# Optimization experiments

Measured on AMD Instinct MI355X. Metric: run time of the kernel, lower is better.

## Reference

```python
import jax, jax.numpy as jnp
import numpy as np

TAU = 1.0
M_OUT = 32  # max_out_node_size
NEG = -1e30


def setup_inputs() -> dict:
    key = jax.random.key(0)
    B, H, U, maxN = 64, 512, 512, 512
    M = M_OUT
    in_size = H + M - 1
    lengths_np = np.where(np.arange(B) % 2 == 0, 256, 512).astype(np.int32)
    total = int(lengths_np.sum())  # 24576
    ks = jax.random.split(key, 14)
    h = jax.random.normal(ks[0], (total, H), jnp.float32)
    hg = jax.random.normal(ks[1], (B, H), jnp.float32)
    u = jax.random.uniform(ks[2], (M, B, maxN), jnp.float32, 1e-20, 1.0)
    gumbel = -jnp.log(-jnp.log(u))
    s = lambda k, shp, fan: jax.random.normal(k, shp, jnp.float32) * (fan ** -0.5)
    return {
        'h': h, 'hg': hg,
        'lengths': jnp.asarray(lengths_np),
        'gumbel': gumbel,
        'W1': s(ks[3], (U, H), H),
        'W2': s(ks[4], (U, H), H),
        'wc': s(ks[5], (U, 1), 1),
        'v': s(ks[6], (1, U), U),
        'w_ih': s(ks[7], (3 * H, in_size), in_size),
        'w_hh': s(ks[8], (3 * H, H), H),
        'b_ih': s(ks[9], (3 * H,), in_size),
        'b_hh': s(ks[10], (3 * H,), in_size),
        'Wf': s(ks[11], (M - 1, H), H),
        'bf': s(ks[12], (M - 1,), H),
    }


def _gru_cell(x, hprev, w_ih, w_hh, b_ih, b_hh):
    H = hprev.shape[-1]
    gi = x @ w_ih.T + b_ih
    gh = hprev @ w_hh.T + b_hh
    r = jax.nn.sigmoid(gi[:, :H] + gh[:, :H])
    z = jax.nn.sigmoid(gi[:, H:2 * H] + gh[:, H:2 * H])
    n = jnp.tanh(gi[:, 2 * H:] + r * gh[:, 2 * H:])
    return (1.0 - z) * n + z * hprev


def reference(h, hg, lengths, gumbel, W1, W2, wc, v, w_ih, w_hh, b_ih, b_hh, Wf, bf):
    B = lengths.shape[0]
    M, _, maxN = gumbel.shape
    H = hg.shape[1]
    total = h.shape[0]
    # pad_sequence: ragged h -> [B, maxN, H], zero-padded
    offsets = jnp.concatenate([jnp.zeros((1,), lengths.dtype), jnp.cumsum(lengths)[:-1]])
    pos = jnp.arange(maxN)
    mask = pos[None, :] < lengths[:, None]                      # [B, maxN]
    idx = jnp.clip(offsets[:, None] + pos[None, :], 0, total - 1)
    enc = h[idx] * mask[..., None].astype(h.dtype)              # [B, maxN, H]
    enc_proj = jnp.einsum('bnh,uh->bnu', enc, W1)               # W1(encoder_out), hoisted
    wc_vec = wc[:, 0]
    v_vec = v[0]
    theta_pos = jnp.arange(M - 1)

    def step(carry, xs):
        dec_in, hid, cov, closs = carry
        g, i = xs
        hid = _gru_cell(dec_in, hid, w_ih, w_hh, b_ih, b_hh)
        uj = jnp.tanh(enc_proj + (hid @ W2.T)[:, None, :] + cov[:, :, None] * wc_vec)
        scores = jnp.einsum('bnu,u->bn', uj, v_vec)
        att = jax.nn.softmax(jnp.where(mask, scores, NEG), axis=-1)  # [B, maxN]
        closs = closs + jnp.minimum(att, cov).sum()
        cov = cov + att
        # gumbel-softmax (hard, straight-through) over nodes
        y = jax.nn.softmax((jnp.log(att + 1e-12) + g) / TAU, axis=1)
        y_hard = jax.nn.one_hot(jnp.argmax(y, axis=1), maxN, dtype=y.dtype)
        att_hard = y_hard + y - jax.lax.stop_gradient(y)
        chosen = jnp.einsum('bnh,bn->bh', enc, att_hard)
        theta = jax.nn.sigmoid(hid @ Wf.T + bf) * (theta_pos < i).astype(hid.dtype)
        dec_in = jnp.concatenate([chosen, theta], axis=1)
        return (dec_in, hid, cov, closs), (att_hard, theta)

    dec_in0 = jnp.zeros((B, H + M - 1), h.dtype)
    cov0 = jnp.zeros((B, maxN), h.dtype)
    carry0 = (dec_in0, hg, cov0, jnp.asarray(0.0, h.dtype))
    (_, _, _, closs), (ptrs, thetas) = jax.lax.scan(step, carry0, (gumbel, jnp.arange(M)))
    pointer = jnp.transpose(ptrs, (1, 2, 0))   # [B, maxN, M]
    adj = jnp.transpose(thetas, (1, 2, 0))     # [B, M-1, M]
    return pointer, closs / B, enc, adj
```

## Files before the change

kernel.cpp:

```cpp
#include <hip/hip_runtime.h>
#include <math.h>

#define B 64
#define H 512
#define MAXN 512
#define U 512
#define MM 32
#define IN_SZ 543
#define DEC_STRIDE 544

#define PTR_OFF 0
#define PTR_SZ (B*MAXN*MM)
#define CLOSS_OFF (PTR_OFF + PTR_SZ)
#define ENC_OFF (CLOSS_OFF + 1)
#define ENC_SZ (B*MAXN*H)
#define ADJ_OFF (ENC_OFF + ENC_SZ)

#define EP_OFF 0
#define EP_SZ (B*MAXN*U)
#define GP_OFF (EP_OFF + EP_SZ)
#define GP_SZ (4*3*B*H)
#define HID0_OFF (GP_OFF + GP_SZ)
#define HID1_OFF (HID0_OFF + B*H)
#define W2H_OFF  (HID1_OFF + B*H)
#define COV_OFF  (W2H_OFF + B*H)
#define SC_OFF   (COV_OFF + B*MAXN)
#define DEC_OFF  (SC_OFF + B*MAXN)
#define CL_OFF   (DEC_OFF + B*DEC_STRIDE)
#define OFFS_OFF (CL_OFF + 64)
#define W1H_OFF  (OFFS_OFF + 64)
#define W1L_OFF  (W1H_OFF + 131072)

typedef short bf16x8 __attribute__((ext_vector_type(8)));
typedef float f32x4  __attribute__((ext_vector_type(4)));

__device__ __forceinline__ float tanh_fast(float x){
    float e = __builtin_amdgcn_exp2f(x * 2.885390081777927f);
    return 1.0f - 2.0f * __builtin_amdgcn_rcpf(e + 1.0f);
}

__device__ __forceinline__ unsigned short f2bf(float x){
    unsigned int u = __float_as_uint(x);
    u = (u + 0x7fffu + ((u >> 16) & 1u)) >> 16;
    return (unsigned short)u;
}

__global__ void k_init(float* __restrict__ ws, float* __restrict__ out,
                       const float* __restrict__ hg, const int* __restrict__ lengths,
                       const float* __restrict__ W1){
    int gid = blockIdx.x*256 + threadIdx.x;
    int nth = gridDim.x*256;
    float* ptr = out + PTR_OFF;
    for (int i=gid;i<PTR_SZ;i+=nth) ptr[i]=0.f;
    float* dec = ws + DEC_OFF;
    for (int i=gid;i<B*DEC_STRIDE;i+=nth) dec[i]=0.f;
    float* cov = ws + COV_OFF;
    float* hid0 = ws + HID0_OFF;
    for (int i=gid;i<B*H;i+=nth){ cov[i]=0.f; hid0[i]=hg[i]; }
    unsigned short* w1h = (unsigned short*)(ws + W1H_OFF);
    unsigned short* w1l = (unsigned short*)(ws + W1L_OFF);
    for (int i=gid;i<512*512;i+=nth){
        float x = W1[i];
        unsigned short hb = f2bf(x);
        float hf = __uint_as_float(((unsigned int)hb)<<16);
        w1h[i] = hb;
        w1l[i] = f2bf(x - hf);
    }
    if (gid<64) (ws+CL_OFF)[gid]=0.f;
    if (gid==0){
        int* offs=(int*)(ws+OFFS_OFF); int acc=0;
        for(int b=0;b<B;b++){ offs[b]=acc; acc+=lengths[b]; }
    }
}

__global__ __launch_bounds__(256) void k_gather(const float* __restrict__ h,
        const int* __restrict__ lengths, const float* __restrict__ offs_f,
        float* __restrict__ enc){
    const int* offs = (const int*)offs_f;
    int t = threadIdx.x;
    int row = blockIdx.x*2 + (t>>7);
    int c = (t&127)*4;
    int b = row >> 9, n = row & 511;
    int len = lengths[b];
    float4 v = make_float4(0.f,0.f,0.f,0.f);
    if (n < len){
        const float* p = h + (size_t)(offs[b]+n)*H + c;
        v = *(const float4*)p;
    }
    float* q = enc + (size_t)row*H + c;
    q[0]=v.x; q[1]=v.y; q[2]=v.z; q[3]=v.w;
}

__global__ __launch_bounds__(256) void k_gemm_mfma(const float* __restrict__ enc,
        const unsigned short* __restrict__ w1h, const unsigned short* __restrict__ w1l,
        float* __restrict__ ep){
    __shared__ unsigned short sAH[128][40];
    __shared__ unsigned short sAL[128][40];
    __shared__ unsigned short sBH[128][40];
    __shared__ unsigned short sBL[128][40];
    int tid = threadIdx.x;
    int bm = blockIdx.x >> 2, bn = blockIdx.x & 3;
    int r0 = bm*128, u0 = bn*128;
    int wid = tid>>6, lane = tid&63;
    int wr = wid>>1, wc = wid&1;
    int lr = lane&15, lk = (lane>>4)*8;
    f32x4 acc[4][4];
#pragma unroll
    for (int i=0;i<4;i++)
#pragma unroll
        for (int j=0;j<4;j++) acc[i][j] = (f32x4){0.f,0.f,0.f,0.f};
    int rowA = tid>>2, seg = tid&3;
    for (int k0=0;k0<512;k0+=32){
#pragma unroll
        for (int half=0; half<2; ++half){
            int row = rowA + half*64;
            const float* asrc = &enc[(size_t)(r0+row)*512 + k0 + seg*8];
            bf16x8 vh, vl;
#pragma unroll
            for (int j=0;j<8;j++){
                float x = asrc[j];
                unsigned short hb = f2bf(x);
                float hf = __uint_as_float(((unsigned int)hb)<<16);
                vh[j] = (short)hb;
                vl[j] = (short)f2bf(x - hf);
            }
            *(bf16x8*)&sAH[row][seg*8] = vh;
            *(bf16x8*)&sAL[row][seg*8] = vl;
            size_t bidx = (size_t)(u0+row)*512 + k0 + seg*8;
            *(bf16x8*)&sBH[row][seg*8] = *(const bf16x8*)&w1h[bidx];
            *(bf16x8*)&sBL[row][seg*8] = *(const bf16x8*)&w1l[bidx];
        }
        __syncthreads();
        bf16x8 aH[4], aL[4], bH[4], bL[4];
#pragma unroll
        for (int f=0; f<4; f++){
            aH[f] = *(const bf16x8*)&sAH[wr*64+f*16+lr][lk];
            aL[f] = *(const bf16x8*)&sAL[wr*64+f*16+lr][lk];
            bH[f] = *(const bf16x8*)&sBH[wc*64+f*16+lr][lk];
            bL[f] = *(const bf16x8*)&sBL[wc*64+f*16+lr][lk];
        }
#pragma unroll
        for (int mf=0;mf<4;mf++){
#pragma unroll
            for (int nf=0;nf<4;nf++){
                acc[mf][nf] = __builtin_amdgcn_mfma_f32_16x16x32_bf16(aH[mf], bH[nf], acc[mf][nf], 0,0,0);
                acc[mf][nf] = __builtin_amdgcn_mfma_f32_16x16x32_bf16(aH[mf], bL[nf], acc[mf][nf], 0,0,0);
                acc[mf][nf] = __builtin_amdgcn_mfma_f32_16x16x32_bf16(aL[mf], bH[nf], acc[mf][nf], 0,0,0);
            }
        }
        __syncthreads();
    }
#pragma unroll
    for (int mf=0;mf<4;mf++){
#pragma unroll
        for (int nf=0;nf<4;nf++){
#pragma unroll
            for (int r=0;r<4;r++){
                int row = r0 + wr*64 + mf*16 + (lane>>4)*4 + r;
                int col = u0 + wc*64 + nf*16 + lr;
                ep[(size_t)row*512 + col] = acc[mf][nf][r];
            }
        }
    }
}

__global__ __launch_bounds__(256) void k_gruP(const float* __restrict__ dec_in,
        const float* __restrict__ hid_in,
        const float* __restrict__ w_ih, const float* __restrict__ w_hh,
        float* __restrict__ gp){
    __shared__ float As[64][36];
    __shared__ float Ws[12][36];
    int tid=threadIdx.x, b=tid&63, q=tid>>6;
    int s = blockIdx.x >> 7;
    int h0 = (int)(blockIdx.x & 127) * 4;
    const float* xs; int xstride, kbeg, kend; const float* W; int wstride;
    if (s==0){ xs=dec_in; xstride=DEC_STRIDE; kbeg=0;   kend=288;   W=w_ih; wstride=IN_SZ; }
    else if(s==1){ xs=dec_in; xstride=DEC_STRIDE; kbeg=288; kend=IN_SZ; W=w_ih; wstride=IN_SZ; }
    else if(s==2){ xs=hid_in; xstride=512; kbeg=0;   kend=256; W=w_hh; wstride=512; }
    else         { xs=hid_in; xstride=512; kbeg=256; kend=512; W=w_hh; wstride=512; }
    float a0=0.f,a1=0.f,a2=0.f;
    for (int k0=kbeg; k0<kend; k0+=32){
        for (int it=0;it<2;it++){
            int idx=tid+it*256; int row=idx>>3, c=idx&7; int k=k0+c*4;
            float4 v=make_float4(0.f,0.f,0.f,0.f);
            const float* p=&xs[row*xstride+k];
            if (k+3 < kend) v=*(const float4*)p;
            else { if(k<kend)v.x=p[0]; if(k+1<kend)v.y=p[1]; if(k+2<kend)v.z=p[2]; }
            *(float4*)&As[row][c*4]=v;
        }
        if (tid<96){
            int rr=tid>>3, c=tid&7; int g=rr>>2, qq=rr&3;
            int j=g*512 + h0+qq; int k=k0+c*4;
            float4 v=make_float4(0.f,0.f,0.f,0.f);
            const float* p=&W[(size_t)j*wstride+k];
            if (wstride==512){
                v=*(const float4*)p;
            } else {
                if(k<kend)v.x=p[0]; if(k+1<kend)v.y=p[1];
                if(k+2<kend)v.z=p[2]; if(k+3<kend)v.w=p[3];
            }
            *(float4*)&Ws[rr][c*4]=v;
        }
        __syncthreads();
#pragma unroll
        for (int kk=0;kk<32;kk+=4){
            float4 a=*(const float4*)&As[b][kk];
            float4 w0=*(const float4*)&Ws[q][kk];
            float4 w1=*(const float4*)&Ws[4+q][kk];
            float4 w2=*(const float4*)&Ws[8+q][kk];
            a0 += a.x*w0.x + a.y*w0.y + a.z*w0.z + a.w*w0.w;
            a1 += a.x*w1.x + a.y*w1.y + a.z*w1.z + a.w*w1.w;
            a2 += a.x*w2.x + a.y*w2.y + a.z*w2.z + a.w*w2.w;
        }
        __syncthreads();
    }
    int h = h0 + q;
    gp[((s*3+0)*64+b)*512 + h] = a0;
    gp[((s*3+1)*64+b)*512 + h] = a1;
    gp[((s*3+2)*64+b)*512 + h] = a2;
}

__global__ __launch_bounds__(512) void k_mid(const float* __restrict__ gp,
        const float* __restrict__ hid_in, float* __restrict__ hid_out,
        const float* __restrict__ b_ih, const float* __restrict__ b_hh,
        const float* __restrict__ W2, const float* __restrict__ Wf,
        const float* __restrict__ bf,
        float* __restrict__ w2h, float* __restrict__ dec_in,
        float* __restrict__ adj, int step){
    __shared__ float sH[512];
    int b = blockIdx.x >> 2, uc = blockIdx.x & 3;
    int tid = threadIdx.x;
    {
        int h = tid;
        float gI0 = gp[((0*3+0)*64+b)*512+h] + gp[((1*3+0)*64+b)*512+h];
        float gI1 = gp[((0*3+1)*64+b)*512+h] + gp[((1*3+1)*64+b)*512+h];
        float gI2 = gp[((0*3+2)*64+b)*512+h] + gp[((1*3+2)*64+b)*512+h];
        float gH0 = gp[((2*3+0)*64+b)*512+h] + gp[((3*3+0)*64+b)*512+h];
        float gH1 = gp[((2*3+1)*64+b)*512+h] + gp[((3*3+1)*64+b)*512+h];
        float gH2 = gp[((2*3+2)*64+b)*512+h] + gp[((3*3+2)*64+b)*512+h];
        float gi0=gI0+b_ih[h],     gh0=gH0+b_hh[h];
        float gi1=gI1+b_ih[512+h], gh1=gH1+b_hh[512+h];
        float gi2=gI2+b_ih[1024+h],gh2=gH2+b_hh[1024+h];
        float r=1.f/(1.f+expf(-(gi0+gh0)));
        float z=1.f/(1.f+expf(-(gi1+gh1)));
        float nn=tanhf(gi2 + r*gh2);
        float hv=(1.f-z)*nn + z*hid_in[b*512+h];
        sH[h]=hv;
        if (uc==0) hid_out[b*512+h]=hv;
    }
    __syncthreads();
    int wv=tid>>6, lane=tid&63;
    for (int ul=wv; ul<128; ul+=8){
        int u = uc*128 + ul;
        const float* wr = &W2[(size_t)u*512];
        float acc=0.f;
#pragma unroll
        for (int t=0;t<8;t++){ int k=t*64+lane; acc += wr[k]*sH[k]; }
#pragma unroll
        for (int m=1;m<64;m<<=1) acc += __shfl_xor(acc, m, 64);
        if (lane==0) w2h[b*512+u]=acc;
    }
    if (uc==0){
        for (int ul=wv; ul<31; ul+=8){
            const float* wr = &Wf[(size_t)ul*512];
            float acc=0.f;
#pragma unroll
            for (int t=0;t<8;t++){ int k=t*64+lane; acc += wr[k]*sH[k]; }
#pragma unroll
            for (int m=1;m<64;m<<=1) acc += __shfl_xor(acc, m, 64);
            if (lane==0){
                float th = 1.f/(1.f+expf(-(acc + bf[ul])));
                th = (ul < step) ? th : 0.f;
                dec_in[b*DEC_STRIDE + 512 + ul] = th;
                adj[b*992 + ul*32 + step] = th;
            }
        }
    }
}

__global__ __launch_bounds__(256) void k_scores(const float* __restrict__ ep,
        const float* __restrict__ w2h, const float* __restrict__ cov,
        const float* __restrict__ wc, const float* __restrict__ v,
        const int* __restrict__ lengths, float* __restrict__ sc){
    __shared__ float sW[512], sV[512], sC[512];
    int b = blockIdx.x >> 4, nc = blockIdx.x & 15;
    int len = lengths[b];
    if (nc*32 >= len) return;
    int tid=threadIdx.x;
    for (int idx=tid; idx<384; idx+=256){
        int which = idx>>7, c = (idx&127)*4;
        float4 val;
        if (which==0) val=*(const float4*)&w2h[b*512+c];
        else if (which==1) val=*(const float4*)&v[c];
        else val=*(const float4*)&wc[c];
        float* dst = (which==0)?sW:((which==1)?sV:sC);
        *(float4*)&dst[c]=val;
    }
    __syncthreads();
    int wv=tid>>6, lane=tid&63;
    float4 vv0=*(const float4*)&sV[lane*8], vv1=*(const float4*)&sV[lane*8+4];
    float4 cc0=*(const float4*)&sC[lane*8], cc1=*(const float4*)&sC[lane*8+4];
    float4 ww0=*(const float4*)&sW[lane*8], ww1=*(const float4*)&sW[lane*8+4];
#pragma unroll
    for (int r=0;r<8;r++){
        int n = nc*32 + wv*8 + r;
        float cb = cov[b*512+n];
        const float4* rr = (const float4*)&ep[((size_t)b*512+n)*512 + lane*8];
        float4 e0=rr[0], e1=rr[1];
        float acc;
        acc  = tanh_fast(e0.x + ww0.x + cb*cc0.x)*vv0.x;
        acc += tanh_fast(e0.y + ww0.y + cb*cc0.y)*vv0.y;
        acc += tanh_fast(e0.z + ww0.z + cb*cc0.z)*vv0.z;
        acc += tanh_fast(e0.w + ww0.w + cb*cc0.w)*vv0.w;
        acc += tanh_fast(e1.x + ww1.x + cb*cc1.x)*vv1.x;
        acc += tanh_fast(e1.y + ww1.y + cb*cc1.y)*vv1.y;
        acc += tanh_fast(e1.z + ww1.z + cb*cc1.z)*vv1.z;
        acc += tanh_fast(e1.w + ww1.w + cb*cc1.w)*vv1.w;
#pragma unroll
        for (int m=1;m<64;m<<=1) acc += __shfl_xor(acc, m, 64);
        if (lane==0) sc[b*512+n]=acc;
    }
}

__global__ __launch_bounds__(512) void k_soft(const float* __restrict__ sc,
        const float* __restrict__ gum, const int* __restrict__ lengths,
        const float* __restrict__ enc, float* __restrict__ cov,
        float* __restrict__ dec_in, float* __restrict__ closs_b,
        float* __restrict__ pointer, int step){
    __shared__ float red[512];
    __shared__ int  redi[512];
    int b=blockIdx.x, n=threadIdx.x;
    int len=lengths[b];
    float e = (n<len)? expf(sc[b*512+n]) : 0.f;
    red[n]=e; __syncthreads();
    for(int o=256;o>=1;o>>=1){ if(n<o) red[n]+=red[n+o]; __syncthreads(); }
    float Z=red[0]; __syncthreads();
    float att=e/Z;
    float c=cov[b*512+n];
    red[n]=fminf(att,c); __syncthreads();
    for(int o=256;o>=1;o>>=1){ if(n<o) red[n]+=red[n+o]; __syncthreads(); }
    if(n==0) closs_b[b]+=red[0];
    __syncthreads();
    cov[b*512+n]=c+att;
    float lg=logf(att+1e-12f)+gum[((size_t)step*64+b)*512+n];
    red[n]=lg; redi[n]=n; __syncthreads();
    for(int o=256;o>=1;o>>=1){
        if(n<o && red[n+o]>red[n]){ red[n]=red[n+o]; redi[n]=redi[n+o]; }
        __syncthreads();
    }
    int ns=redi[0];
    if(n==0) pointer[b*16384 + ns*32 + step]=1.f;
    dec_in[b*DEC_STRIDE+n]=enc[((size_t)b*512+ns)*512+n];
}

__global__ void k_final(const float* __restrict__ closs_b, float* __restrict__ out){
    if (threadIdx.x==0 && blockIdx.x==0){
        float s=0.f;
        for(int b=0;b<B;b++) s+=closs_b[b];
        out[CLOSS_OFF]=s/64.f;
    }
}

extern "C" void kernel_launch(void* const* d_in, const int* in_sizes, int n_in,
                              void* d_out, int out_size, void* d_ws, size_t ws_size,
                              hipStream_t stream){
    const float* h      = (const float*)d_in[0];
    const float* hg     = (const float*)d_in[1];
    const int*   lengths= (const int*)  d_in[2];
    const float* gumbel = (const float*)d_in[3];
    const float* W1     = (const float*)d_in[4];
    const float* W2     = (const float*)d_in[5];
    const float* wc     = (const float*)d_in[6];
    const float* v      = (const float*)d_in[7];
    const float* w_ih   = (const float*)d_in[8];
    const float* w_hh   = (const float*)d_in[9];
    const float* b_ih   = (const float*)d_in[10];
    const float* b_hh   = (const float*)d_in[11];
    const float* Wf     = (const float*)d_in[12];
    const float* bf     = (const float*)d_in[13];
    float* out = (float*)d_out;
    float* ws  = (float*)d_ws;
    float* enc = out + ENC_OFF;
    float* adj = out + ADJ_OFF;
    float* pointer = out + PTR_OFF;
    float* ep   = ws + EP_OFF;
    float* gp   = ws + GP_OFF;
    float* hidA = ws + HID0_OFF;
    float* hidB = ws + HID1_OFF;
    float* w2h  = ws + W2H_OFF;
    float* cov  = ws + COV_OFF;
    float* sc   = ws + SC_OFF;
    float* dec  = ws + DEC_OFF;
    float* clb  = ws + CL_OFF;
    const unsigned short* w1h = (const unsigned short*)(ws + W1H_OFF);
    const unsigned short* w1l = (const unsigned short*)(ws + W1L_OFF);

    hipLaunchKernelGGL(k_init,     dim3(512),  dim3(256), 0, stream, ws, out, hg, lengths, W1);
    hipLaunchKernelGGL(k_gather,   dim3(16384),dim3(256), 0, stream, h, lengths, ws+OFFS_OFF, enc);
    hipLaunchKernelGGL(k_gemm_mfma,dim3(1024), dim3(256), 0, stream, enc, w1h, w1l, ep);

    for (int i=0;i<MM;i++){
        const float* hin = (i&1)? hidB : hidA;
        float*       hout= (i&1)? hidA : hidB;
        hipLaunchKernelGGL(k_gruP,   dim3(512),  dim3(256), 0, stream,
                           dec, hin, w_ih, w_hh, gp);
        hipLaunchKernelGGL(k_mid,    dim3(256),  dim3(512), 0, stream,
                           gp, hin, hout, b_ih, b_hh, W2, Wf, bf, w2h, dec, adj, i);
        hipLaunchKernelGGL(k_scores, dim3(1024), dim3(256), 0, stream,
                           ep, w2h, cov, wc, v, lengths, sc);
        hipLaunchKernelGGL(k_soft,   dim3(64),   dim3(512), 0, stream,
                           sc, gumbel, lengths, enc, cov, dec, clb, pointer, i);
    }
    hipLaunchKernelGGL(k_final, dim3(1), dim3(64), 0, stream, clb, out);
}
```

Before: 1.732 ms.

## Fuse gumbel argmax and coverage update into next step's GRU projection kernel

Moves the per-step softmax/gumbel argmax, coverage update and pointer write from a separate kernel into the following iteration's GRU input-projection kernel. Each input-side block redundantly recomputes the selected node for all batch rows and gathers the chosen encoder row and theta directly into shared memory, removing the dec_in buffer. This cuts one kernel launch per decoding step at the cost of duplicated reduction work and extra score/gumbel reads per block. The last step's selection is handled by a single trailing launch of the old kernel.

```diff
diff --git a/kernel.cpp b/kernel.cpp
--- a/kernel.cpp
+++ b/kernel.cpp
@@ -26,7 +26,8 @@
 #define COV_OFF  (W2H_OFF + B*H)
 #define SC_OFF   (COV_OFF + B*MAXN)
 #define DEC_OFF  (SC_OFF + B*MAXN)
-#define CL_OFF   (DEC_OFF + B*DEC_STRIDE)
+#define TH_OFF   (DEC_OFF + B*DEC_STRIDE)
+#define CL_OFF   (TH_OFF + B*32)
 #define OFFS_OFF (CL_OFF + 64)
 #define W1H_OFF  (OFFS_OFF + 64)
 #define W1L_OFF  (W1H_OFF + 131072)
@@ -52,8 +53,6 @@
     int nth = gridDim.x*256;
     float* ptr = out + PTR_OFF;
     for (int i=gid;i<PTR_SZ;i+=nth) ptr[i]=0.f;
-    float* dec = ws + DEC_OFF;
-    for (int i=gid;i<B*DEC_STRIDE;i+=nth) dec[i]=0.f;
     float* cov = ws + COV_OFF;
     float* hid0 = ws + HID0_OFF;
     for (int i=gid;i<B*H;i+=nth){ cov[i]=0.f; hid0[i]=hg[i]; }
@@ -164,29 +163,109 @@
     }
 }
 
-__global__ __launch_bounds__(256) void k_gruP(const float* __restrict__ dec_in,
+__global__ __launch_bounds__(256) void k_gruPS(
         const float* __restrict__ hid_in,
         const float* __restrict__ w_ih, const float* __restrict__ w_hh,
-        float* __restrict__ gp){
+        const float* __restrict__ sc, const float* __restrict__ gum,
+        const int* __restrict__ lengths, const float* __restrict__ enc,
+        const float* __restrict__ th, float* __restrict__ cov,
+        float* __restrict__ clb, float* __restrict__ pointer,
+        float* __restrict__ gp, int step){
     __shared__ float As[64][36];
     __shared__ float Ws[12][36];
+    __shared__ float red[256];
+    __shared__ int   sNs[64];
+    __shared__ float sZ[64];
     int tid=threadIdx.x, b=tid&63, q=tid>>6;
     int s = blockIdx.x >> 7;
-    int h0 = (int)(blockIdx.x & 127) * 4;
-    const float* xs; int xstride, kbeg, kend; const float* W; int wstride;
-    if (s==0){ xs=dec_in; xstride=DEC_STRIDE; kbeg=0;   kend=288;   W=w_ih; wstride=IN_SZ; }
-    else if(s==1){ xs=dec_in; xstride=DEC_STRIDE; kbeg=288; kend=IN_SZ; W=w_ih; wstride=IN_SZ; }
-    else if(s==2){ xs=hid_in; xstride=512; kbeg=0;   kend=256; W=w_hh; wstride=512; }
-    else         { xs=hid_in; xstride=512; kbeg=256; kend=512; W=w_hh; wstride=512; }
+    int hc = blockIdx.x & 127;
+    int h0 = hc * 4;
+
+    if (s < 2 && step > 0){
+        int wv = tid>>6, lane = tid&63;
+        for (int bb=wv; bb<64; bb+=4){
+            int len = lengths[bb];
+            const float* scb = &sc[bb*512];
+            const float* gb  = &gum[((size_t)(step-1)*64+bb)*512];
+            float e[8]; float zs=0.f;
+#pragma unroll
+            for (int c=0;c<8;c++){
+                int n = c*64 + lane;
+                float ev = (n<len)? expf(scb[n]) : 0.f;
+                e[c]=ev; zs += ev;
+            }
+#pragma unroll
+            for (int m=1;m<64;m<<=1) zs += __shfl_xor(zs, m, 64);
+            float best=-1e38f; int bi=0;
+#pragma unroll
+            for (int c=0;c<8;c++){
+                int n = c*64 + lane;
+                float lg = logf(e[c]/zs + 1e-12f) + gb[n];
+                if (lg > best){ best=lg; bi=n; }
+            }
+#pragma unroll
+            for (int m=1;m<64;m<<=1){
+                float ob = __shfl_xor(best, m, 64);
+                int   oi = __shfl_xor(bi, m, 64);
+                if (ob > best || (ob==best && oi<bi)){ best=ob; bi=oi; }
+            }
+            if (lane==0){ sNs[bb]=bi; sZ[bb]=zs; }
+        }
+        __syncthreads();
+        if (s==0 && hc < 64){
+            int bb = hc;
+            int len = lengths[bb];
+            float Z = sZ[bb];
+            int n0=tid, n1=tid+256;
+            float e0=(n0<len)? expf(sc[bb*512+n0]) : 0.f;
+            float e1=(n1<len)? expf(sc[bb*512+n1]) : 0.f;
+            float a0=e0/Z, a1=e1/Z;
+            float c0=cov[bb*512+n0], c1=cov[bb*512+n1];
+            red[tid]=fminf(a0,c0)+fminf(a1,c1); __syncthreads();
+            for(int o=128;o>=1;o>>=1){ if(tid<o) red[tid]+=red[tid+o]; __syncthreads(); }
+            if(tid==0){
+                clb[bb] += red[0];
+                pointer[bb*16384 + sNs[bb]*32 + (step-1)] = 1.f;
+            }
+            cov[bb*512+n0]=c0+a0;
+            cov[bb*512+n1]=c1+a1;
+            __syncthreads();
+        }
+    }
+
+    int kbeg, kend; const float* W; int wstride;
+    if (s==0){ kbeg=0;   kend=288;   W=w_ih; wstride=IN_SZ; }
+    else if(s==1){ kbeg=288; kend=IN_SZ; W=w_ih; wstride=IN_SZ; }
+    else if(s==2){ kbeg=0;   kend=256; W=w_hh; wstride=512; }
+    else         { kbeg=256; kend=512; W=w_hh; wstride=512; }
     float a0=0.f,a1=0.f,a2=0.f;
     for (int k0=kbeg; k0<kend; k0+=32){
-        for (int it=0;it<2;it++){
-            int idx=tid+it*256; int row=idx>>3, c=idx&7; int k=k0+c*4;
-            float4 v=make_float4(0.f,0.f,0.f,0.f);
-            const float* p=&xs[row*xstride+k];
-            if (k+3 < kend) v=*(const float4*)p;
-            else { if(k<kend)v.x=p[0]; if(k+1<kend)v.y=p[1]; if(k+2<kend)v.z=p[2]; }
-            *(float4*)&As[row][c*4]=v;
+        if (s < 2){
+            for (int it=0;it<2;it++){
+                int idx=tid+it*256; int row=idx>>3, c=idx&7; int k=k0+c*4;
+                float vx0=0.f, vx1=0.f, vx2=0.f, vx3=0.f;
+                if (step > 0){
+                    int nsr = sNs[row];
+                    const float* er = &enc[((size_t)(row*512 + nsr))*512];
+                    const float* tr = &th[row*32];
+#pragma unroll
+                    for (int j=0;j<4;j++){
+                        int kk = k + j;
+                        float val;
+                        if (kk < 512) val = er[kk];
+                        else if (kk < IN_SZ) val = tr[kk-512];
+                        else val = 0.f;
+                        if (j==0) vx0=val; else if(j==1) vx1=val;
+                        else if (j==2) vx2=val; else vx3=val;
+                    }
+                }
+                *(float4*)&As[row][c*4]=make_float4(vx0,vx1,vx2,vx3);
+            }
+        } else {
+            for (int it=0;it<2;it++){
+                int idx=tid+it*256; int row=idx>>3,c=idx&7; int k=k0+c*4;
+                *(float4*)&As[row][c*4] = *(const float4*)&hid_in[row*512+k];
+            }
         }
         if (tid<96){
             int rr=tid>>3, c=tid&7; int g=rr>>2, qq=rr&3;
@@ -225,7 +304,7 @@
         const float* __restrict__ b_ih, const float* __restrict__ b_hh,
         const float* __restrict__ W2, const float* __restrict__ Wf,
         const float* __restrict__ bf,
-        float* __restrict__ w2h, float* __restrict__ dec_in,
+        float* __restrict__ w2h, float* __restrict__ th,
         float* __restrict__ adj, int step){
     __shared__ float sH[512];
     int b = blockIdx.x >> 2, uc = blockIdx.x & 3;
@@ -269,10 +348,10 @@
 #pragma unroll
             for (int m=1;m<64;m<<=1) acc += __shfl_xor(acc, m, 64);
             if (lane==0){
-                float th = 1.f/(1.f+expf(-(acc + bf[ul])));
-                th = (ul < step) ? th : 0.f;
-                dec_in[b*DEC_STRIDE + 512 + ul] = th;
-                adj[b*992 + ul*32 + step] = th;
+                float thv = 1.f/(1.f+expf(-(acc + bf[ul])));
+                thv = (ul < step) ? thv : 0.f;
+                th[b*32 + ul] = thv;
+                adj[b*992 + ul*32 + step] = thv;
             }
         }
     }
@@ -391,6 +470,7 @@
     float* cov  = ws + COV_OFF;
     float* sc   = ws + SC_OFF;
     float* dec  = ws + DEC_OFF;
+    float* th   = ws + TH_OFF;
     float* clb  = ws + CL_OFF;
     const unsigned short* w1h = (const unsigned short*)(ws + W1H_OFF);
     const unsigned short* w1l = (const unsigned short*)(ws + W1L_OFF);
@@ -402,14 +482,15 @@
     for (int i=0;i<MM;i++){
         const float* hin = (i&1)? hidB : hidA;
         float*       hout= (i&1)? hidA : hidB;
-        hipLaunchKernelGGL(k_gruP,   dim3(512),  dim3(256), 0, stream,
-                           dec, hin, w_ih, w_hh, gp);
+        hipLaunchKernelGGL(k_gruPS,  dim3(512),  dim3(256), 0, stream,
+                           hin, w_ih, w_hh, sc, gumbel, lengths, enc, th,
+                           cov, clb, pointer, gp, i);
         hipLaunchKernelGGL(k_mid,    dim3(256),  dim3(512), 0, stream,
-                           gp, hin, hout, b_ih, b_hh, W2, Wf, bf, w2h, dec, adj, i);
+                           gp, hin, hout, b_ih, b_hh, W2, Wf, bf, w2h, th, adj, i);
         hipLaunchKernelGGL(k_scores, dim3(1024), dim3(256), 0, stream,
                            ep, w2h, cov, wc, v, lengths, sc);
-        hipLaunchKernelGGL(k_soft,   dim3(64),   dim3(512), 0, stream,
-                           sc, gumbel, lengths, enc, cov, dec, clb, pointer, i);
-    }
-    hipLaunchKernelGGL(k_final, dim3(1), dim3(64), 0, stream, clb, out);
-}
+    }
+    hipLaunchKernelGGL(k_soft,  dim3(64), dim3(512), 0, stream,
+                       sc, gumbel, lengths, enc, cov, dec, clb, pointer, MM-1);
+    hipLaunchKernelGGL(k_final, dim3(1),  dim3(64),  0, stream, clb, out);
+}
```

Measured after the change: 3.340 ms. 92.9% more time.

## Fuse attention score computation with softmax and gumbel argmax kernel

Applied to the files above, without the earlier changes.

Merges the per-step attention-score kernel and the softmax/coverage/argmax kernel into one kernel with a single 1024-thread block per batch row. Scores and coverage now stay in shared memory instead of going through a global scratch buffer, and one launch per decoder step is removed. The cost is that the score computation, which streams about 1MB of the projected encoder per batch row, drops from 1024 blocks to 64. That leaves most of the GPU idle during the bandwidth- and tanh-heavy phase.

```diff
diff --git a/kernel.cpp b/kernel.cpp
--- a/kernel.cpp
+++ b/kernel.cpp
@@ -24,8 +24,7 @@
 #define HID1_OFF (HID0_OFF + B*H)
 #define W2H_OFF  (HID1_OFF + B*H)
 #define COV_OFF  (W2H_OFF + B*H)
-#define SC_OFF   (COV_OFF + B*MAXN)
-#define DEC_OFF  (SC_OFF + B*MAXN)
+#define DEC_OFF  (COV_OFF + B*MAXN)
 #define CL_OFF   (DEC_OFF + B*DEC_STRIDE)
 #define OFFS_OFF (CL_OFF + 64)
 #define W1H_OFF  (OFFS_OFF + 64)
@@ -278,79 +277,88 @@
     }
 }
 
-__global__ __launch_bounds__(256) void k_scores(const float* __restrict__ ep,
-        const float* __restrict__ w2h, const float* __restrict__ cov,
+__global__ __launch_bounds__(1024) void k_scsoft(
+        const float* __restrict__ ep, const float* __restrict__ w2h,
         const float* __restrict__ wc, const float* __restrict__ v,
-        const int* __restrict__ lengths, float* __restrict__ sc){
-    __shared__ float sW[512], sV[512], sC[512];
-    int b = blockIdx.x >> 4, nc = blockIdx.x & 15;
-    int len = lengths[b];
-    if (nc*32 >= len) return;
-    int tid=threadIdx.x;
-    for (int idx=tid; idx<384; idx+=256){
-        int which = idx>>7, c = (idx&127)*4;
-        float4 val;
-        if (which==0) val=*(const float4*)&w2h[b*512+c];
-        else if (which==1) val=*(const float4*)&v[c];
-        else val=*(const float4*)&wc[c];
-        float* dst = (which==0)?sW:((which==1)?sV:sC);
-        *(float4*)&dst[c]=val;
-    }
-    __syncthreads();
-    int wv=tid>>6, lane=tid&63;
-    float4 vv0=*(const float4*)&sV[lane*8], vv1=*(const float4*)&sV[lane*8+4];
-    float4 cc0=*(const float4*)&sC[lane*8], cc1=*(const float4*)&sC[lane*8+4];
-    float4 ww0=*(const float4*)&sW[lane*8], ww1=*(const float4*)&sW[lane*8+4];
-#pragma unroll
-    for (int r=0;r<8;r++){
-        int n = nc*32 + wv*8 + r;
-        float cb = cov[b*512+n];
-        const float4* rr = (const float4*)&ep[((size_t)b*512+n)*512 + lane*8];
-        float4 e0=rr[0], e1=rr[1];
-        float acc;
-        acc  = tanh_fast(e0.x + ww0.x + cb*cc0.x)*vv0.x;
-        acc += tanh_fast(e0.y + ww0.y + cb*cc0.y)*vv0.y;
-        acc += tanh_fast(e0.z + ww0.z + cb*cc0.z)*vv0.z;
-        acc += tanh_fast(e0.w + ww0.w + cb*cc0.w)*vv0.w;
-        acc += tanh_fast(e1.x + ww1.x + cb*cc1.x)*vv1.x;
-        acc += tanh_fast(e1.y + ww1.y + cb*cc1.y)*vv1.y;
-        acc += tanh_fast(e1.z + ww1.z + cb*cc1.z)*vv1.z;
-        acc += tanh_fast(e1.w + ww1.w + cb*cc1.w)*vv1.w;
-#pragma unroll
-        for (int m=1;m<64;m<<=1) acc += __shfl_xor(acc, m, 64);
-        if (lane==0) sc[b*512+n]=acc;
-    }
-}
-
-__global__ __launch_bounds__(512) void k_soft(const float* __restrict__ sc,
-        const float* __restrict__ gum, const int* __restrict__ lengths,
-        const float* __restrict__ enc, float* __restrict__ cov,
-        float* __restrict__ dec_in, float* __restrict__ closs_b,
-        float* __restrict__ pointer, int step){
+        const int* __restrict__ lengths, const float* __restrict__ gum,
+        const float* __restrict__ enc,
+        float* __restrict__ cov, float* __restrict__ dec_in,
+        float* __restrict__ closs_b, float* __restrict__ pointer, int step){
+    __shared__ float sW[512], sV[512], sC[512], sCov[512];
+    __shared__ float sSc[512];
     __shared__ float red[512];
     __shared__ int  redi[512];
-    int b=blockIdx.x, n=threadIdx.x;
-    int len=lengths[b];
-    float e = (n<len)? expf(sc[b*512+n]) : 0.f;
-    red[n]=e; __syncthreads();
-    for(int o=256;o>=1;o>>=1){ if(n<o) red[n]+=red[n+o]; __syncthreads(); }
-    float Z=red[0]; __syncthreads();
-    float att=e/Z;
-    float c=cov[b*512+n];
-    red[n]=fminf(att,c); __syncthreads();
-    for(int o=256;o>=1;o>>=1){ if(n<o) red[n]+=red[n+o]; __syncthreads(); }
-    if(n==0) closs_b[b]+=red[0];
-    __syncthreads();
-    cov[b*512+n]=c+att;
-    float lg=logf(att+1e-12f)+gum[((size_t)step*64+b)*512+n];
-    red[n]=lg; redi[n]=n; __syncthreads();
-    for(int o=256;o>=1;o>>=1){
-        if(n<o && red[n+o]>red[n]){ red[n]=red[n+o]; redi[n]=redi[n+o]; }
+    const int b = blockIdx.x, tid = threadIdx.x;
+    const int wv = tid>>6, lane = tid&63;
+    const int len = lengths[b];
+
+    {
+        int seg = tid >> 7, off = (tid & 127) * 4;
+        if (seg==0)      *(float4*)&sW[off]   = *(const float4*)&w2h[b*512+off];
+        else if (seg==1) *(float4*)&sV[off]   = *(const float4*)&v[off];
+        else if (seg==2) *(float4*)&sC[off]   = *(const float4*)&wc[off];
+        else if (seg==3) *(float4*)&sCov[off] = *(const float4*)&cov[b*512+off];
+        else if (seg==4) { if ((tid&127)<128) *(float4*)&sSc[off] = make_float4(0.f,0.f,0.f,0.f); }
+    }
+    __syncthreads();
+
+    {
+        float4 vv0=*(const float4*)&sV[lane*8], vv1=*(const float4*)&sV[lane*8+4];
+        float4 cc0=*(const float4*)&sC[lane*8], cc1=*(const float4*)&sC[lane*8+4];
+        float4 ww0=*(const float4*)&sW[lane*8], ww1=*(const float4*)&sW[lane*8+4];
+        int rows = len >> 4;
+#pragma unroll 4
+        for (int r=0; r<rows; ++r){
+            int n = r*16 + wv;
+            float cb = sCov[n];
+            const float4* rr = (const float4*)&ep[((size_t)b*512+n)*512 + lane*8];
+            float4 e0=rr[0], e1=rr[1];
+            float acc;
+            acc  = tanh_fast(e0.x + ww0.x + cb*cc0.x)*vv0.x;
+            acc += tanh_fast(e0.y + ww0.y + cb*cc0.y)*vv0.y;
+            acc += tanh_fast(e0.z + ww0.z + cb*cc0.z)*vv0.z;
+            acc += tanh_fast(e0.w + ww0.w + cb*cc0.w)*vv0.w;
+            acc += tanh_fast(e1.x + ww1.x + cb*cc1.x)*vv1.x;
+            acc += tanh_fast(e1.y + ww1.y + cb*cc1.y)*vv1.y;
+            acc += tanh_fast(e1.z + ww1.z + cb*cc1.z)*vv1.z;
+            acc += tanh_fast(e1.w + ww1.w + cb*cc1.w)*vv1.w;
+#pragma unroll
+            for (int m=1;m<64;m<<=1) acc += __shfl_xor(acc, m, 64);
+            if (lane==0) sSc[n]=acc;
+        }
+    }
+    __syncthreads();
+
+    int n = tid;
+    float e = 0.f;
+    if (n < 512){ e = (n < len) ? expf(sSc[n]) : 0.f; red[n] = e; }
+    __syncthreads();
+    for (int o=256;o>=1;o>>=1){ if (n<o) red[n]+=red[n+o]; __syncthreads(); }
+    float Z = red[0];
+    __syncthreads();
+    float att = 0.f, cvo = 0.f;
+    if (n < 512){
+        att = e / Z;
+        cvo = sCov[n];
+        red[n] = fminf(att, cvo);
+    }
+    __syncthreads();
+    for (int o=256;o>=1;o>>=1){ if (n<o) red[n]+=red[n+o]; __syncthreads(); }
+    if (tid==0) closs_b[b] += red[0];
+    __syncthreads();
+    if (n < 512){
+        cov[b*512+n] = cvo + att;
+        float lg = logf(att + 1e-12f) + gum[((size_t)step*64+b)*512 + n];
+        red[n] = lg; redi[n] = n;
+    }
+    __syncthreads();
+    for (int o=256;o>=1;o>>=1){
+        if (n<o && red[n+o]>red[n]){ red[n]=red[n+o]; redi[n]=redi[n+o]; }
         __syncthreads();
     }
-    int ns=redi[0];
-    if(n==0) pointer[b*16384 + ns*32 + step]=1.f;
-    dec_in[b*DEC_STRIDE+n]=enc[((size_t)b*512+ns)*512+n];
+    int ns = redi[0];
+    if (tid==0) pointer[b*16384 + ns*32 + step] = 1.f;
+    if (n < 512) dec_in[b*DEC_STRIDE + n] = enc[((size_t)b*512+ns)*512 + n];
 }
 
 __global__ void k_final(const float* __restrict__ closs_b, float* __restrict__ out){
@@ -389,7 +397,6 @@
     float* hidB = ws + HID1_OFF;
     float* w2h  = ws + W2H_OFF;
     float* cov  = ws + COV_OFF;
-    float* sc   = ws + SC_OFF;
     float* dec  = ws + DEC_OFF;
     float* clb  = ws + CL_OFF;
     const unsigned short* w1h = (const unsigned short*)(ws + W1H_OFF);
@@ -402,14 +409,13 @@
     for (int i=0;i<MM;i++){
         const float* hin = (i&1)? hidB : hidA;
         float*       hout= (i&1)? hidA : hidB;
-        hipLaunchKernelGGL(k_gruP,   dim3(512),  dim3(256), 0, stream,
+        hipLaunchKernelGGL(k_gruP,   dim3(512), dim3(256),  0, stream,
                            dec, hin, w_ih, w_hh, gp);
-        hipLaunchKernelGGL(k_mid,    dim3(256),  dim3(512), 0, stream,
+        hipLaunchKernelGGL(k_mid,    dim3(256), dim3(512),  0, stream,
                            gp, hin, hout, b_ih, b_hh, W2, Wf, bf, w2h, dec, adj, i);
-        hipLaunchKernelGGL(k_scores, dim3(1024), dim3(256), 0, stream,
-                           ep, w2h, cov, wc, v, lengths, sc);
-        hipLaunchKernelGGL(k_soft,   dim3(64),   dim3(512), 0, stream,
-                           sc, gumbel, lengths, enc, cov, dec, clb, pointer, i);
+        hipLaunchKernelGGL(k_scsoft, dim3(64),  dim3(1024), 0, stream,
+                           ep, w2h, wc, v, lengths, gumbel, enc,
+                           cov, dec, clb, pointer, i);
     }
     hipLaunchKernelGGL(k_final, dim3(1), dim3(64), 0, stream, clb, out);
 }
```

Result: slower. 2.092 ms (+20.8%).
